# Kernel tuning notes

Hardware: AMD Instinct MI355X
Metric: run time of the kernel (lower is better)

## Reference

```python
import jax, jax.numpy as jnp
import numpy as np

B, V, G, D = 16, 16384, 20000, 64


def setup_inputs() -> dict:
    key = jax.random.key(0)
    k1, k2 = jax.random.split(key)
    variant_embeddings = jax.random.normal(k1, (B, V, D), dtype=jnp.float32)
    gene_ids = jax.random.randint(k2, (B, V), 0, G, dtype=jnp.int64)
    mask = jnp.ones((B, V), dtype=bool)
    return {
        "variant_embeddings": variant_embeddings,
        "gene_ids": gene_ids,
        "mask": mask,
        "num_genes": G,
    }


def reference(variant_embeddings, gene_ids, mask, num_genes):
    # Aggregation = 'max'. Genes with no valid variants -> zero embedding.
    b, v, d = variant_embeddings.shape
    # Flatten (batch, variant) and build per-(batch,gene) segment ids.
    seg = (jnp.arange(b, dtype=gene_ids.dtype)[:, None] * num_genes + gene_ids).reshape(-1)
    m = mask.reshape(-1)
    # Route padded variants to a dummy trailing segment so they never contribute.
    dummy = b * num_genes
    seg = jnp.where(m, seg, dummy)
    x = variant_embeddings.reshape(b * v, d)  # mask-zeroing is a no-op for selected (valid) rows under max
    num_segments = b * num_genes + 1
    mx = jax.ops.segment_max(x, seg, num_segments=num_segments)[: b * num_genes]  # [b*G, d]
    counts = jax.ops.segment_sum(m.astype(x.dtype), seg, num_segments=num_segments)[: b * num_genes]  # [b*G]
    out = jnp.where(counts[:, None] > 0, mx, jnp.zeros((), dtype=x.dtype))
    return out.reshape(b, num_genes, d)
```

## Files before the change

kernel.cpp:

```cpp
#include <hip/hip_runtime.h>

constexpr int B = 16;
constexpr int V = 16384;
constexpr int G = 20000;
constexpr int D = 64;
constexpr int NCELLS = B * G;
constexpr int NROWS  = B * V;
constexpr int OVF_MAX = 16384;
constexpr long long OUT_N = (long long)NCELLS * D;

typedef float f32x4 __attribute__((ext_vector_type(4)));

constexpr int HDR_WORDS = 4 * NCELLS;
constexpr int OVF_HDR   = HDR_WORDS;
constexpr int OVF_LIST  = HDR_WORDS + 1;
constexpr int SPILL_OFF = HDR_WORDS + 1 + 2 * OVF_MAX;

__global__ void ga_zero(uint4* __restrict__ ws4, unsigned int* __restrict__ ws) {
  int stride = gridDim.x * blockDim.x;
  for (int i = blockIdx.x * blockDim.x + threadIdx.x; i < HDR_WORDS / 4; i += stride)
    ws4[i] = make_uint4(0u, 0u, 0u, 0u);
  if (blockIdx.x == 0 && threadIdx.x == 0) ws[OVF_HDR] = 0u;
}

__global__ void ga_build(const int* __restrict__ gene_ids,
                         const int* __restrict__ mask,
                         unsigned int* __restrict__ ws, int scap) {
  int r = blockIdx.x * blockDim.x + threadIdx.x;
  if (r >= NROWS) return;
  if (!mask[r]) return;
  int cell = (r >> 14) * G + gene_ids[r];
  unsigned int pos = atomicAdd(&ws[cell * 4], 1u);
  if (pos < 3u) {
    ws[cell * 4 + 1 + pos] = (unsigned int)r;
  } else if (pos < 3u + (unsigned int)scap) {
    ws[SPILL_OFF + (size_t)cell * scap + (pos - 3u)] = (unsigned int)r;
  } else {
    unsigned int o = atomicAdd(&ws[OVF_HDR], 1u);
    if (o < (unsigned int)OVF_MAX) {
      ws[OVF_LIST + 2 * o + 0] = (unsigned int)cell;
      ws[OVF_LIST + 2 * o + 1] = (unsigned int)r;
    }
  }
}

__device__ __forceinline__ void fmax4(f32x4& a, f32x4 v) {
  a.x = fmaxf(a.x, v.x);
  a.y = fmaxf(a.y, v.y);
  a.z = fmaxf(a.z, v.z);
  a.w = fmaxf(a.w, v.w);
}

constexpr int CPT = 8;
__global__ void ga_gather(const f32x4* __restrict__ emb4,
                          const uint4* __restrict__ hdr,
                          const unsigned int* __restrict__ spill,
                          f32x4* __restrict__ out4, int scap) {
  const int STRIDE = NCELLS / CPT;
  int t = blockIdx.x * blockDim.x + threadIdx.x;
  int cell0 = t >> 4;
  int sub   = t & 15;
  if (cell0 >= STRIDE) return;

  uint4 h[CPT];
#pragma unroll
  for (int k = 0; k < CPT; ++k)
    h[k] = hdr[cell0 + k * STRIDE];

  f32x4 v0[CPT];
#pragma unroll
  for (int k = 0; k < CPT; ++k) {
    unsigned int row = h[k].x ? h[k].y : 0u;
    v0[k] = emb4[(size_t)row * 16 + sub];
  }

#pragma unroll
  for (int k = 0; k < CPT; ++k) {
    int cell = cell0 + k * STRIDE;
    unsigned int c = h[k].x;
    f32x4 acc = v0[k];
    if (c >= 2u) fmax4(acc, emb4[(size_t)h[k].z * 16 + sub]);
    if (c >= 3u) fmax4(acc, emb4[(size_t)h[k].w * 16 + sub]);
    if (c > 3u) {
      int n1 = (int)c - 3; if (n1 > scap) n1 = scap;
      const unsigned int* sp = spill + (size_t)cell * scap;
      for (int j = 0; j < n1; ++j)
        fmax4(acc, emb4[(size_t)sp[j] * 16 + sub]);
    }
    if (c == 0u) acc = (f32x4)(0.f);
    __builtin_nontemporal_store(acc, &out4[(size_t)cell * 16 + sub]);
  }
}

__device__ __forceinline__ void atomic_max_float(float* addr, float val) {
  unsigned int* ua = (unsigned int*)addr;
  unsigned int old = *ua;
  while (__uint_as_float(old) < val) {
    unsigned int assumed = old;
    old = atomicCAS(ua, assumed, __float_as_uint(val));
    if (old == assumed) break;
  }
}

__global__ void ga_ovf(const f32x4* __restrict__ emb4,
                       const unsigned int* __restrict__ ws,
                       float* __restrict__ out) {
  unsigned int nov = ws[OVF_HDR];
  if (nov > (unsigned int)OVF_MAX) nov = OVF_MAX;
  int total = (int)nov * 16;
  int stride = gridDim.x * blockDim.x;
  for (int u = blockIdx.x * blockDim.x + threadIdx.x; u < total; u += stride) {
    int e = u >> 4, sub = u & 15;
    unsigned int cell = ws[OVF_LIST + 2 * e + 0];
    unsigned int row  = ws[OVF_LIST + 2 * e + 1];
    f32x4 v = emb4[(size_t)row * 16 + sub];
    float* o = out + (size_t)cell * 64 + sub * 4;
    atomic_max_float(o + 0, v.x);
    atomic_max_float(o + 1, v.y);
    atomic_max_float(o + 2, v.z);
    atomic_max_float(o + 3, v.w);
  }
}

__device__ __forceinline__ unsigned int enc_f32(float f) {
  unsigned int u = __float_as_uint(f);
  return (u & 0x80000000u) ? ~u : (u | 0x80000000u);
}
__device__ __forceinline__ float dec_f32(unsigned int e) {
  unsigned int u = (e & 0x80000000u) ? (e ^ 0x80000000u) : ~e;
  return __uint_as_float(u);
}

__global__ void ga_init(uint4* __restrict__ out4, int n4) {
  int stride = gridDim.x * blockDim.x;
  for (int i = blockIdx.x * blockDim.x + threadIdx.x; i < n4; i += stride)
    out4[i] = make_uint4(0u, 0u, 0u, 0u);
}

__global__ void ga_scatter(const float4* __restrict__ emb4,
                           const int* __restrict__ gene_ids,
                           const int* __restrict__ mask,
                           unsigned int* __restrict__ out) {
  int tid = blockIdx.x * blockDim.x + threadIdx.x;
  int v  = tid >> 4;
  int dq = tid & 15;
  if (!mask[v]) return;
  int g = gene_ids[v];
  int b = v >> 14;
  float4 e = emb4[tid];
  int base = (b * G + g) * D + (dq << 2);
  atomicMax(out + base + 0, enc_f32(e.x));
  atomicMax(out + base + 1, enc_f32(e.y));
  atomicMax(out + base + 2, enc_f32(e.z));
  atomicMax(out + base + 3, enc_f32(e.w));
}

__global__ void ga_finalize(uint4* __restrict__ io4, int n4) {
  int stride = gridDim.x * blockDim.x;
  for (int i = blockIdx.x * blockDim.x + threadIdx.x; i < n4; i += stride) {
    uint4 e = io4[i];
    float4 f;
    f.x = e.x ? dec_f32(e.x) : 0.0f;
    f.y = e.y ? dec_f32(e.y) : 0.0f;
    f.z = e.z ? dec_f32(e.z) : 0.0f;
    f.w = e.w ? dec_f32(e.w) : 0.0f;
    *reinterpret_cast<float4*>(io4 + i) = f;
  }
}

extern "C" void kernel_launch(void* const* d_in, const int* in_sizes, int n_in,
                              void* d_out, int out_size, void* d_ws, size_t ws_size,
                              hipStream_t stream) {
  const float4* emb4     = (const float4*)d_in[0];
  const int*    gene_ids = (const int*)d_in[1];
  const int*    mask     = (const int*)d_in[2];

  long long ws_u32 = (long long)(ws_size / 4);
  long long avail  = ws_u32 - (long long)SPILL_OFF;
  int scap = (int)(avail > 0 ? avail / NCELLS : -1);
  if (scap > 13) scap = 13;

  if (scap >= 0) {
    unsigned int* ws = (unsigned int*)d_ws;
    ga_zero<<<1024, 256, 0, stream>>>((uint4*)d_ws, ws);
    ga_build<<<NROWS / 256, 256, 0, stream>>>(gene_ids, mask, ws, scap);
    const int N = (NCELLS / CPT) * 16;
    ga_gather<<<N / 256, 256, 0, stream>>>(
        (const f32x4*)emb4, (const uint4*)d_ws, ws + SPILL_OFF,
        (f32x4*)d_out, scap);
    ga_ovf<<<64, 256, 0, stream>>>((const f32x4*)emb4, ws, (float*)d_out);
  } else {
    unsigned int* out_u = (unsigned int*)d_out;
    const int n4 = (int)(OUT_N / 4);
    ga_init<<<2048, 256, 0, stream>>>((uint4*)d_out, n4);
    ga_scatter<<<(NROWS * 16) / 256, 256, 0, stream>>>(emb4, gene_ids, mask, out_u);
    ga_finalize<<<2048, 256, 0, stream>>>((uint4*)d_out, n4);
  }
}
```

Baseline: 50.35 us.

## Classify cells by count into compacted lists and process singletons separately

Adds a classify pass that compacts cells into lists of single-variant cells (with their row) and multi-variant cells. The output is zero-filled in bulk, singleton cells are copied directly, and only multi-variant cells run the max-reduction kernel. This replaces one uniform gather kernel whose warps diverged on per-cell counts. In exchange it adds three more kernel launches, an extra full write of the output for the zero fill, and a dependency on the compacted list counts.

```diff
diff --git a/kernel.cpp b/kernel.cpp
--- a/kernel.cpp
+++ b/kernel.cpp
@@ -14,13 +14,15 @@
 constexpr int HDR_WORDS = 4 * NCELLS;
 constexpr int OVF_HDR   = HDR_WORDS;
 constexpr int OVF_LIST  = HDR_WORDS + 1;
-constexpr int SPILL_OFF = HDR_WORDS + 1 + 2 * OVF_MAX;
-
-__global__ void ga_zero(uint4* __restrict__ ws4, unsigned int* __restrict__ ws) {
-  int stride = gridDim.x * blockDim.x;
-  for (int i = blockIdx.x * blockDim.x + threadIdx.x; i < HDR_WORDS / 4; i += stride)
-    ws4[i] = make_uint4(0u, 0u, 0u, 0u);
-  if (blockIdx.x == 0 && threadIdx.x == 0) ws[OVF_HDR] = 0u;
+constexpr int LCNT_OFF  = OVF_LIST + 2 * OVF_MAX;
+constexpr int C1_OFF    = (LCNT_OFF + 2 + 1) & ~1;
+constexpr int C2_OFF    = C1_OFF + 2 * NCELLS;
+constexpr int SPILL_OFF = C2_OFF + NCELLS;
+
+__global__ void ga_zero(unsigned int* __restrict__ ws) {
+  int i = blockIdx.x * blockDim.x + threadIdx.x;
+  if (i < NCELLS) reinterpret_cast<uint4*>(ws)[i] = make_uint4(0u, 0u, 0u, 0u);
+  if (i == 0) { ws[OVF_HDR] = 0u; ws[LCNT_OFF] = 0u; ws[LCNT_OFF + 1] = 0u; }
 }
 
 __global__ void ga_build(const int* __restrict__ gene_ids,
@@ -44,6 +46,51 @@
   }
 }
 
+__global__ void ga_classify(const uint4* __restrict__ hdr,
+                            unsigned int* __restrict__ ws) {
+  __shared__ unsigned int n1, n2, b1, b2;
+  int cell = blockIdx.x * 256 + threadIdx.x;
+  if (threadIdx.x == 0) { n1 = 0u; n2 = 0u; }
+  __syncthreads();
+  uint4 h = hdr[cell];
+  unsigned int s1 = 0u, s2 = 0u;
+  if (h.x == 1u)      s1 = atomicAdd(&n1, 1u);
+  else if (h.x >= 2u) s2 = atomicAdd(&n2, 1u);
+  __syncthreads();
+  if (threadIdx.x == 0) {
+    b1 = atomicAdd(&ws[LCNT_OFF],     n1);
+    b2 = atomicAdd(&ws[LCNT_OFF + 1], n2);
+  }
+  __syncthreads();
+  if (h.x == 1u)
+    reinterpret_cast<uint2*>(ws + C1_OFF)[b1 + s1] = make_uint2((unsigned)cell, h.y);
+  else if (h.x >= 2u)
+    ws[C2_OFF + b2 + s2] = (unsigned)cell;
+}
+
+__global__ void ga_fill(f32x4* __restrict__ out4) {
+  long long stride = (long long)gridDim.x * blockDim.x;
+  for (long long i = blockIdx.x * (long long)blockDim.x + threadIdx.x;
+       i < OUT_N / 4; i += stride)
+    __builtin_nontemporal_store((f32x4)(0.f), &out4[i]);
+}
+
+__global__ void ga_c1(const f32x4* __restrict__ emb4,
+                      const unsigned int* __restrict__ ws,
+                      f32x4* __restrict__ out4) {
+  unsigned int n = ws[LCNT_OFF];
+  const uint2* lst = reinterpret_cast<const uint2*>(ws + C1_OFF);
+  long long total  = (long long)n * 16;
+  long long stride = (long long)gridDim.x * blockDim.x;
+  for (long long u = blockIdx.x * (long long)blockDim.x + threadIdx.x;
+       u < total; u += stride) {
+    int i = (int)(u >> 4), sub = (int)(u & 15);
+    uint2 e = lst[i];
+    f32x4 v = emb4[(size_t)e.y * 16 + sub];
+    __builtin_nontemporal_store(v, &out4[(size_t)e.x * 16 + sub]);
+  }
+}
+
 __device__ __forceinline__ void fmax4(f32x4& a, f32x4 v) {
   a.x = fmaxf(a.x, v.x);
   a.y = fmaxf(a.y, v.y);
@@ -51,43 +98,29 @@
   a.w = fmaxf(a.w, v.w);
 }
 
-constexpr int CPT = 8;
-__global__ void ga_gather(const f32x4* __restrict__ emb4,
-                          const uint4* __restrict__ hdr,
-                          const unsigned int* __restrict__ spill,
-                          f32x4* __restrict__ out4, int scap) {
-  const int STRIDE = NCELLS / CPT;
-  int t = blockIdx.x * blockDim.x + threadIdx.x;
-  int cell0 = t >> 4;
-  int sub   = t & 15;
-  if (cell0 >= STRIDE) return;
-
-  uint4 h[CPT];
-#pragma unroll
-  for (int k = 0; k < CPT; ++k)
-    h[k] = hdr[cell0 + k * STRIDE];
-
-  f32x4 v0[CPT];
-#pragma unroll
-  for (int k = 0; k < CPT; ++k) {
-    unsigned int row = h[k].x ? h[k].y : 0u;
-    v0[k] = emb4[(size_t)row * 16 + sub];
-  }
-
-#pragma unroll
-  for (int k = 0; k < CPT; ++k) {
-    int cell = cell0 + k * STRIDE;
-    unsigned int c = h[k].x;
-    f32x4 acc = v0[k];
-    if (c >= 2u) fmax4(acc, emb4[(size_t)h[k].z * 16 + sub]);
-    if (c >= 3u) fmax4(acc, emb4[(size_t)h[k].w * 16 + sub]);
-    if (c > 3u) {
-      int n1 = (int)c - 3; if (n1 > scap) n1 = scap;
+__global__ void ga_c2p(const f32x4* __restrict__ emb4,
+                       const uint4* __restrict__ hdr,
+                       const unsigned int* __restrict__ ws,
+                       f32x4* __restrict__ out4, int scap) {
+  unsigned int n = ws[LCNT_OFF + 1];
+  const unsigned int* lst   = ws + C2_OFF;
+  const unsigned int* spill = ws + SPILL_OFF;
+  long long total  = (long long)n * 16;
+  long long stride = (long long)gridDim.x * blockDim.x;
+  for (long long u = blockIdx.x * (long long)blockDim.x + threadIdx.x;
+       u < total; u += stride) {
+    int i = (int)(u >> 4), sub = (int)(u & 15);
+    unsigned int cell = lst[i];
+    uint4 h = hdr[cell];
+    f32x4 acc = emb4[(size_t)h.y * 16 + sub];
+    fmax4(acc, emb4[(size_t)h.z * 16 + sub]);
+    if (h.x >= 3u) fmax4(acc, emb4[(size_t)h.w * 16 + sub]);
+    if (h.x > 3u) {
+      int n1 = (int)h.x - 3; if (n1 > scap) n1 = scap;
       const unsigned int* sp = spill + (size_t)cell * scap;
       for (int j = 0; j < n1; ++j)
         fmax4(acc, emb4[(size_t)sp[j] * 16 + sub]);
     }
-    if (c == 0u) acc = (f32x4)(0.f);
     __builtin_nontemporal_store(acc, &out4[(size_t)cell * 16 + sub]);
   }
 }
@@ -180,14 +213,15 @@
   int scap = (int)(avail > 0 ? avail / NCELLS : -1);
   if (scap > 13) scap = 13;
 
-  if (scap >= 0) {
+  if (scap >= 1) {
     unsigned int* ws = (unsigned int*)d_ws;
-    ga_zero<<<1024, 256, 0, stream>>>((uint4*)d_ws, ws);
+    ga_zero<<<(NCELLS + 255) / 256, 256, 0, stream>>>(ws);
     ga_build<<<NROWS / 256, 256, 0, stream>>>(gene_ids, mask, ws, scap);
-    const int N = (NCELLS / CPT) * 16;
-    ga_gather<<<N / 256, 256, 0, stream>>>(
-        (const f32x4*)emb4, (const uint4*)d_ws, ws + SPILL_OFF,
-        (f32x4*)d_out, scap);
+    ga_classify<<<NCELLS / 256, 256, 0, stream>>>((const uint4*)d_ws, ws);
+    ga_fill<<<2048, 256, 0, stream>>>((f32x4*)d_out);
+    ga_c1<<<8192, 256, 0, stream>>>((const f32x4*)emb4, ws, (f32x4*)d_out);
+    ga_c2p<<<2048, 256, 0, stream>>>((const f32x4*)emb4, (const uint4*)d_ws,
+                                     ws, (f32x4*)d_out, scap);
     ga_ovf<<<64, 256, 0, stream>>>((const f32x4*)emb4, ws, (float*)d_out);
   } else {
     unsigned int* out_u = (unsigned int*)d_out;
```

Result: slower. 95.00 us (+88.7%).

## Split gather into coalesced singleton scatter and multi-row cell pass

Applied to the files above, without the earlier changes.

Cells holding exactly one row are now written by a row-ordered scatter kernel that reads embeddings contiguously and copies them straight to the output. A per-cell kernel handles only empty cells (writing zeros) and cells with two or more rows, replacing the 8-cell-per-thread gather. The custom zero kernel becomes hipMemsetAsync. This adds a kernel launch and a second read of the header and gene ids, in exchange for sequential embedding reads in place of random gathers for most cells.

```diff
diff --git a/kernel.cpp b/kernel.cpp
--- a/kernel.cpp
+++ b/kernel.cpp
@@ -14,14 +14,7 @@
 constexpr int HDR_WORDS = 4 * NCELLS;
 constexpr int OVF_HDR   = HDR_WORDS;
 constexpr int OVF_LIST  = HDR_WORDS + 1;
-constexpr int SPILL_OFF = HDR_WORDS + 1 + 2 * OVF_MAX;
-
-__global__ void ga_zero(uint4* __restrict__ ws4, unsigned int* __restrict__ ws) {
-  int stride = gridDim.x * blockDim.x;
-  for (int i = blockIdx.x * blockDim.x + threadIdx.x; i < HDR_WORDS / 4; i += stride)
-    ws4[i] = make_uint4(0u, 0u, 0u, 0u);
-  if (blockIdx.x == 0 && threadIdx.x == 0) ws[OVF_HDR] = 0u;
-}
+constexpr int SPILL_OFF = OVF_LIST + 2 * OVF_MAX;
 
 __global__ void ga_build(const int* __restrict__ gene_ids,
                          const int* __restrict__ mask,
@@ -44,6 +37,21 @@
   }
 }
 
+__global__ void ga_scatter1(const f32x4* __restrict__ emb4,
+                            const int* __restrict__ gene_ids,
+                            const int* __restrict__ mask,
+                            const unsigned int* __restrict__ ws,
+                            f32x4* __restrict__ out4) {
+  int tid = blockIdx.x * blockDim.x + threadIdx.x;
+  int row = tid >> 4;
+  int sub = tid & 15;
+  if (!mask[row]) return;
+  int cell = (row >> 14) * G + gene_ids[row];
+  if (ws[cell * 4] != 1u) return;
+  f32x4 v = emb4[tid];
+  __builtin_nontemporal_store(v, &out4[(size_t)cell * 16 + sub]);
+}
+
 __device__ __forceinline__ void fmax4(f32x4& a, f32x4 v) {
   a.x = fmaxf(a.x, v.x);
   a.y = fmaxf(a.y, v.y);
@@ -51,45 +59,28 @@
   a.w = fmaxf(a.w, v.w);
 }
 
-constexpr int CPT = 8;
-__global__ void ga_gather(const f32x4* __restrict__ emb4,
-                          const uint4* __restrict__ hdr,
-                          const unsigned int* __restrict__ spill,
-                          f32x4* __restrict__ out4, int scap) {
-  const int STRIDE = NCELLS / CPT;
+__global__ void ga_c2(const f32x4* __restrict__ emb4,
+                      const uint4* __restrict__ hdr,
+                      const unsigned int* __restrict__ spill,
+                      f32x4* __restrict__ out4, int scap) {
   int t = blockIdx.x * blockDim.x + threadIdx.x;
-  int cell0 = t >> 4;
-  int sub   = t & 15;
-  if (cell0 >= STRIDE) return;
-
-  uint4 h[CPT];
-#pragma unroll
-  for (int k = 0; k < CPT; ++k)
-    h[k] = hdr[cell0 + k * STRIDE];
-
-  f32x4 v0[CPT];
-#pragma unroll
-  for (int k = 0; k < CPT; ++k) {
-    unsigned int row = h[k].x ? h[k].y : 0u;
-    v0[k] = emb4[(size_t)row * 16 + sub];
-  }
-
-#pragma unroll
-  for (int k = 0; k < CPT; ++k) {
-    int cell = cell0 + k * STRIDE;
-    unsigned int c = h[k].x;
-    f32x4 acc = v0[k];
-    if (c >= 2u) fmax4(acc, emb4[(size_t)h[k].z * 16 + sub]);
-    if (c >= 3u) fmax4(acc, emb4[(size_t)h[k].w * 16 + sub]);
-    if (c > 3u) {
-      int n1 = (int)c - 3; if (n1 > scap) n1 = scap;
+  int cell = t >> 4;
+  int sub  = t & 15;
+  uint4 h = hdr[cell];
+  if (h.x == 1u) return;
+  f32x4 acc = (f32x4)(0.f);
+  if (h.x >= 2u) {
+    acc = emb4[(size_t)h.y * 16 + sub];
+    fmax4(acc, emb4[(size_t)h.z * 16 + sub]);
+    if (h.x >= 3u) fmax4(acc, emb4[(size_t)h.w * 16 + sub]);
+    if (h.x > 3u) {
+      int n1 = (int)h.x - 3; if (n1 > scap) n1 = scap;
       const unsigned int* sp = spill + (size_t)cell * scap;
       for (int j = 0; j < n1; ++j)
         fmax4(acc, emb4[(size_t)sp[j] * 16 + sub]);
     }
-    if (c == 0u) acc = (f32x4)(0.f);
-    __builtin_nontemporal_store(acc, &out4[(size_t)cell * 16 + sub]);
   }
+  __builtin_nontemporal_store(acc, &out4[(size_t)cell * 16 + sub]);
 }
 
 __device__ __forceinline__ void atomic_max_float(float* addr, float val) {
@@ -180,12 +171,13 @@
   int scap = (int)(avail > 0 ? avail / NCELLS : -1);
   if (scap > 13) scap = 13;
 
-  if (scap >= 0) {
+  if (scap >= 1) {
     unsigned int* ws = (unsigned int*)d_ws;
-    ga_zero<<<1024, 256, 0, stream>>>((uint4*)d_ws, ws);
+    hipMemsetAsync(d_ws, 0, (size_t)(HDR_WORDS + 1) * 4, stream);
     ga_build<<<NROWS / 256, 256, 0, stream>>>(gene_ids, mask, ws, scap);
-    const int N = (NCELLS / CPT) * 16;
-    ga_gather<<<N / 256, 256, 0, stream>>>(
+    ga_scatter1<<<NROWS * 16 / 256, 256, 0, stream>>>(
+        (const f32x4*)emb4, gene_ids, mask, ws, (f32x4*)d_out);
+    ga_c2<<<NCELLS * 16 / 256, 256, 0, stream>>>(
         (const f32x4*)emb4, (const uint4*)d_ws, ws + SPILL_OFF,
         (f32x4*)d_out, scap);
     ga_ovf<<<64, 256, 0, stream>>>((const f32x4*)emb4, ws, (float*)d_out);
```

After: 63.38 us. 25.9% more time.
